# Kernel optimization log

Hardware: AMD Instinct MI355X
Metric: run time of the kernel (lower is better)

The kernel has to match this reference:

```python
import jax, jax.numpy as jnp
import numpy as np

B, S, E, H = 2, 2048, 1024, 16
D = E // H  # head_dim = 64


def setup_inputs() -> dict:
    key = jax.random.key(0)
    ks = jax.random.split(key, 7)
    scale = 1.0 / np.sqrt(E)
    return {
        "q": jax.random.normal(ks[0], (B, S, E), jnp.float32),
        "k": jax.random.normal(ks[1], (B, S, E), jnp.float32),
        "v": jax.random.normal(ks[2], (B, S, E), jnp.float32),
        "Wq": jax.random.normal(ks[3], (E, E), jnp.float32) * scale,
        "bq": jnp.zeros((E,), jnp.float32),
        "Wk": jax.random.normal(ks[4], (E, E), jnp.float32) * scale,
        "bk": jnp.zeros((E,), jnp.float32),
        "Wv": jax.random.normal(ks[5], (E, E), jnp.float32) * scale,
        "bv": jnp.zeros((E,), jnp.float32),
        "Wo": jax.random.normal(ks[6], (E, E), jnp.float32) * scale,
        "bo": jnp.zeros((E,), jnp.float32),
    }


def _split_heads(x):
    # [B, S, E] -> [B, H, S, D]
    b, s, _ = x.shape
    return x.reshape(b, s, H, D).transpose(0, 2, 1, 3)


def reference(q, k, v, Wq, bq, Wk, bk, Wv, bv, Wo, bo):
    qh = _split_heads(q @ Wq + bq)  # [B,H,S,D]
    kh = _split_heads(k @ Wk + bk)
    vh = _split_heads(v @ Wv + bv)
    scores = jnp.einsum("bhqd,bhkd->bhqk", qh, kh) / jnp.sqrt(jnp.float32(D))
    # causal mask, TF band_part(ones, -1, 0) == lower triangular
    mask = jnp.tril(jnp.ones((S, S), jnp.float32))
    scores = scores * mask - 1e9 * (1.0 - mask)
    weights = jax.nn.softmax(scores, axis=-1)
    attn = jnp.einsum("bhqk,bhkd->bhqd", weights, vh)  # [B,H,S,D]
    concat = attn.transpose(0, 2, 1, 3).reshape(q.shape[0], S, E)
    return concat @ Wo + bo
```

## Files before the change

### kernel.cpp

```cpp
#include <hip/hip_runtime.h>
#include <math.h>

#define Bd 2
#define Sd 2048
#define Ed 1024
#define Hd 16
#define Dd 64
#define Md (Bd * Sd)
#define Kd 1024
#define Nd 1024

typedef __attribute__((ext_vector_type(8))) short bf16x8;
typedef __attribute__((ext_vector_type(4))) float f32x4;

__device__ __forceinline__ unsigned short f2bf(float f) {
    unsigned x = __float_as_uint(f);
    x += 0x7fffu + ((x >> 16) & 1u);
    return (unsigned short)(x >> 16);
}

__device__ __forceinline__ unsigned pk_bf16_rhu(float a, float b) {
    return __builtin_amdgcn_perm(__float_as_uint(b) + 0x8000u,
                                 __float_as_uint(a) + 0x8000u, 0x07060302u);
}

__device__ __forceinline__ void gl2lds16(const unsigned short* g, unsigned short* l) {
    __builtin_amdgcn_global_load_lds(
        (__attribute__((address_space(1))) void*)g,
        (__attribute__((address_space(3))) void*)l, 16, 0, 0);
}

__global__ __launch_bounds__(256) void prep_k(
    const float* __restrict__ q, const float* __restrict__ k, const float* __restrict__ v,
    unsigned short* __restrict__ qb, unsigned short* __restrict__ kb,
    unsigned short* __restrict__ vb,
    const float* __restrict__ w0, const float* __restrict__ w1,
    const float* __restrict__ w2, const float* __restrict__ w3,
    unsigned short* __restrict__ o0, unsigned short* __restrict__ o1,
    unsigned short* __restrict__ o2, unsigned short* __restrict__ o3)
{
    const int bx = blockIdx.x;
    if (bx < 3072) {
        const int zz = bx >> 10;
        const int blk = bx & 1023;
        const float* s = zz == 0 ? q : zz == 1 ? k : v;
        unsigned short* d = zz == 0 ? qb : zz == 1 ? kb : vb;
        const int n4 = (Bd * Sd * Ed) / 4;
        int i = blk * 256 + threadIdx.x;
        for (; i < n4; i += 1024 * 256) {
            float4 x = ((const float4*)s)[i];
            uint2 u = make_uint2(pk_bf16_rhu(x.x, x.y), pk_bf16_rhu(x.z, x.w));
            ((uint2*)d)[i] = u;
        }
        return;
    }
    __shared__ unsigned short Tl[32][36];
    const int idx = bx - 3072;
    const int z   = idx >> 10;
    const int ky  = (idx >> 5) & 31;
    const int nx  = idx & 31;
    const float* W = z == 0 ? w0 : z == 1 ? w1 : z == 2 ? w2 : w3;
    unsigned short* Wt = z == 0 ? o0 : z == 1 ? o1 : z == 2 ? o2 : o3;

    const int t = threadIdx.x;
    const int r = t >> 3;
    const int c4 = (t & 7) * 4;
    const int k0 = ky * 32;
    const int n0 = nx * 32;

    float4 x = *(const float4*)(W + (size_t)(k0 + r) * Nd + n0 + c4);
    Tl[c4 + 0][r] = f2bf(x.x);
    Tl[c4 + 1][r] = f2bf(x.y);
    Tl[c4 + 2][r] = f2bf(x.z);
    Tl[c4 + 3][r] = f2bf(x.w);
    __syncthreads();
    ushort4 u = make_ushort4(Tl[r][c4 + 0], Tl[r][c4 + 1], Tl[r][c4 + 2], Tl[r][c4 + 3]);
    *(ushort4*)(Wt + (size_t)(n0 + r) * Kd + k0 + c4) = u;
}

template <int AM>
__device__ __forceinline__ void gemm_v5(
    const unsigned short* __restrict__ A, const unsigned short* __restrict__ Bt,
    const float* __restrict__ bias, void* __restrict__ Yv,
    int m0, int n0, int mode, float oscale)
{
    constexpr int AMT = AM / 32;
    __shared__ unsigned short As[2][AM * 32];
    __shared__ unsigned short Bs[2][128 * 32];

    const int tid  = threadIdx.x;
    const int w    = tid >> 6;
    const int lane = tid & 63;
    const int ln   = lane & 15;
    const int quad = lane >> 4;
    const int wm = (w >> 1) * (AM / 2);
    const int wn = (w & 1) * 64;

    const int lrow = lane >> 2;
    const int lcol = (lane & 3) * 8;

    const unsigned short* Bg0 = Bt + (size_t)(n0 + (2 * w) * 16 + lrow) * Kd + lcol;
    const unsigned short* Bg1 = Bg0 + 16 * Kd;
    const int aseg = (AM == 128) ? 2 * w : w;
    const unsigned short* Ag0 = A + (size_t)(m0 + aseg * 16 + lrow) * Kd + lcol;
    const unsigned short* Ag1 = Ag0 + 16 * Kd;

    f32x4 acc[AMT][4];
    #pragma unroll
    for (int i = 0; i < AMT; ++i)
        #pragma unroll
        for (int j = 0; j < 4; ++j)
            acc[i][j] = (f32x4){0.f, 0.f, 0.f, 0.f};

    gl2lds16(Bg0, &Bs[0][(2 * w) * 512]);
    gl2lds16(Bg1, &Bs[0][(2 * w) * 512 + 512]);
    gl2lds16(Ag0, &As[0][aseg * 512]);
    if constexpr (AM == 128) gl2lds16(Ag1, &As[0][aseg * 512 + 512]);

    for (int k0 = 0; k0 < Kd; k0 += 32) {
        const int buf = (k0 >> 5) & 1;
        __syncthreads();

        if (k0 + 32 < Kd) {
            gl2lds16(Bg0 + k0 + 32, &Bs[buf ^ 1][(2 * w) * 512]);
            gl2lds16(Bg1 + k0 + 32, &Bs[buf ^ 1][(2 * w) * 512 + 512]);
            gl2lds16(Ag0 + k0 + 32, &As[buf ^ 1][aseg * 512]);
            if constexpr (AM == 128)
                gl2lds16(Ag1 + k0 + 32, &As[buf ^ 1][aseg * 512 + 512]);
        }

        bf16x8 af[AMT], bfr[4];
        #pragma unroll
        for (int mi = 0; mi < AMT; ++mi)
            af[mi] = *(const bf16x8*)(&As[buf][(wm + mi * 16 + ln) * 32 + quad * 8]);
        #pragma unroll
        for (int ni = 0; ni < 4; ++ni)
            bfr[ni] = *(const bf16x8*)(&Bs[buf][(wn + ni * 16 + ln) * 32 + quad * 8]);
        #pragma unroll
        for (int mi = 0; mi < AMT; ++mi)
            #pragma unroll
            for (int ni = 0; ni < 4; ++ni)
                acc[mi][ni] = __builtin_amdgcn_mfma_f32_16x16x32_bf16(
                    af[mi], bfr[ni], acc[mi][ni], 0, 0, 0);
    }

    float bval[4];
    #pragma unroll
    for (int ni = 0; ni < 4; ++ni) bval[ni] = bias[n0 + wn + ni * 16 + ln];

    if (mode == 0) {
        float* Y = (float*)Yv;
        #pragma unroll
        for (int mi = 0; mi < AMT; ++mi) {
            #pragma unroll
            for (int ni = 0; ni < 4; ++ni) {
                int n = n0 + wn + ni * 16 + ln;
                #pragma unroll
                for (int r = 0; r < 4; ++r) {
                    int m = m0 + wm + mi * 16 + quad * 4 + r;
                    Y[(size_t)m * Nd + n] = (acc[mi][ni][r] + bval[ni]) * oscale;
                }
            }
        }
    } else if (mode == 1) {
        unsigned short* Y = (unsigned short*)Yv;
        #pragma unroll
        for (int mi = 0; mi < AMT; ++mi) {
            #pragma unroll
            for (int ni = 0; ni < 4; ++ni) {
                int n = n0 + wn + ni * 16 + ln;
                int h = n >> 6, d = n & 63;
                #pragma unroll
                for (int r = 0; r < 4; ++r) {
                    int m = m0 + wm + mi * 16 + quad * 4 + r;
                    int b = m >> 11, s = m & 2047;
                    Y[(((size_t)b * Hd + h) * Sd + s) * Dd + d] =
                        f2bf((acc[mi][ni][r] + bval[ni]) * oscale);
                }
            }
        }
    } else {
        unsigned short* Y = (unsigned short*)Yv;
        #pragma unroll
        for (int mi = 0; mi < AMT; ++mi) {
            int mbase = m0 + wm + mi * 16 + quad * 4;
            int b = mbase >> 11, s = mbase & 2047;
            #pragma unroll
            for (int ni = 0; ni < 4; ++ni) {
                int n = n0 + wn + ni * 16 + ln;
                int h = n >> 6, d = n & 63;
                ushort4 u = make_ushort4(
                    f2bf((acc[mi][ni][0] + bval[ni]) * oscale),
                    f2bf((acc[mi][ni][1] + bval[ni]) * oscale),
                    f2bf((acc[mi][ni][2] + bval[ni]) * oscale),
                    f2bf((acc[mi][ni][3] + bval[ni]) * oscale));
                *(ushort4*)(Y + (((size_t)b * Hd + h) * Dd + d) * Sd + s) = u;
            }
        }
    }
}

__global__ __launch_bounds__(256) void proj_gemm_k(
    const unsigned short* A0, const unsigned short* A1, const unsigned short* A2,
    const unsigned short* B0, const unsigned short* B1, const unsigned short* B2,
    const float* b0, const float* b1, const float* b2,
    unsigned short* Y0, unsigned short* Y1, unsigned short* Y2)
{
    const int l    = blockIdx.x;
    const int xcd  = l & 7;
    const int g    = l >> 3;
    const int n_t  = g & 7;
    const int msub = (g >> 3) & 3;
    const int z    = g >> 5;
    const int m_t  = xcd * 4 + msub;

    const unsigned short* A = z == 0 ? A0 : z == 1 ? A1 : A2;
    const unsigned short* B = z == 0 ? B0 : z == 1 ? B1 : B2;
    const float* bias       = z == 0 ? b0 : z == 1 ? b1 : b2;
    unsigned short* Y       = z == 0 ? Y0 : z == 1 ? Y1 : Y2;
    gemm_v5<128>(A, B, bias, Y, m_t * 128, n_t * 128,
                 z == 2 ? 2 : 1,
                 z == 0 ? 0.18033688011112042f : 1.0f);
}

__global__ __launch_bounds__(256) void out_gemm_k(
    const unsigned short* A, const unsigned short* Bt, const float* bias, float* Y)
{
    const int l    = blockIdx.x;
    const int xcd  = l & 7;
    const int g    = l >> 3;
    const int n_t  = g & 7;
    const int msub = g >> 3;
    const int m_t  = xcd * 8 + msub;
    gemm_v5<64>(A, Bt, bias, Y, m_t * 64, n_t * 128, 0, 1.0f);
}

__global__ __launch_bounds__(256) void attn_mfma_k(
    const unsigned short* __restrict__ Qg,
    const unsigned short* __restrict__ Kg,
    const unsigned short* __restrict__ Vg,
    unsigned short* __restrict__ Aout)
{
    __shared__ unsigned short Ks[2][2][64 * 64];
    __shared__ unsigned short Vs[2][2][64 * 64];
    __shared__ unsigned short Pt[4][16][72];

    const int tid  = threadIdx.x;
    const int w    = tid >> 6;
    const int lane = tid & 63;
    const int ln   = lane & 15;
    const int quad = lane >> 4;

    const int l   = blockIdx.x;
    const int bh  = (l & 7) * 4 + ((l >> 3) & 3);
    const int qtA = l >> 5;
    const int b   = bh >> 4;
    const int h   = bh & 15;

    const size_t baseQK = (size_t)bh * Sd * Dd;
    const size_t baseV  = (size_t)bh * Dd * Sd;
    const f32x4 vzero = {0.f, 0.f, 0.f, 0.f};

    const int qtB = 31 - qtA;
    const int nA  = qtA + 1;

    const int sr = lane >> 3;
    const int sc = ((lane & 7) ^ sr) * 8;
    const int rb0 = w * 16, rb1 = w * 16 + 8;
    const int swl = ln & 7;
    const int c0 = ((quad    ) ^ swl) * 8;
    const int c1 = ((quad + 4) ^ swl) * 8;

    const int qrowA = qtA * 64 + w * 16;
    const int qrowB = qtB * 64 + w * 16;
    const unsigned short* qpA = Qg + baseQK + (size_t)(qrowA + ln) * Dd + 8 * quad;
    const unsigned short* qpB = Qg + baseQK + (size_t)(qrowB + ln) * Dd + 8 * quad;
    const bf16x8 qA0 = *(const bf16x8*)(qpA), qA1 = *(const bf16x8*)(qpA + 32);
    const bf16x8 qB0 = *(const bf16x8*)(qpB), qB1 = *(const bf16x8*)(qpB + 32);

    float l_lane = 0.f;
    f32x4 O[4];
    #pragma unroll
    for (int t = 0; t < 4; ++t) O[t] = vzero;

    #pragma unroll
    for (int s = 0; s < 2; ++s) {
        const int ts = s;
        const int nk = ((ts < nA) ? ts : ts - nA) * 64;
        gl2lds16(Kg + baseQK + (size_t)(nk + rb0 + sr) * Dd + sc, &Ks[0][s][rb0 * 64]);
        gl2lds16(Kg + baseQK + (size_t)(nk + rb1 + sr) * Dd + sc, &Ks[0][s][rb1 * 64]);
        gl2lds16(Vg + baseV  + (size_t)(rb0 + sr) * Sd + nk + sc, &Vs[0][s][rb0 * 64]);
        gl2lds16(Vg + baseV  + (size_t)(rb1 + sr) * Sd + nk + sc, &Vs[0][s][rb1 * 64]);
    }

    for (int g = 0; g < 17; ++g) {
        const int cur = g & 1;
        __syncthreads();

        if (g + 1 < 17) {
            #pragma unroll
            for (int s = 0; s < 2; ++s) {
                const int ts = 2 * (g + 1) + s;
                if (ts < 33) {
                    const int nk = ((ts < nA) ? ts : ts - nA) * 64;
                    gl2lds16(Kg + baseQK + (size_t)(nk + rb0 + sr) * Dd + sc,
                             &Ks[cur ^ 1][s][rb0 * 64]);
                    gl2lds16(Kg + baseQK + (size_t)(nk + rb1 + sr) * Dd + sc,
                             &Ks[cur ^ 1][s][rb1 * 64]);
                    gl2lds16(Vg + baseV  + (size_t)(rb0 + sr) * Sd + nk + sc,
                             &Vs[cur ^ 1][s][rb0 * 64]);
                    gl2lds16(Vg + baseV  + (size_t)(rb1 + sr) * Sd + nk + sc,
                             &Vs[cur ^ 1][s][rb1 * 64]);
                }
            }
        }

        #pragma unroll
        for (int s = 0; s < 2; ++s) {
            const int it = 2 * g + s;
            if (it >= 33) break;

            const bool inA   = (it < nA);
            const int  krow  = (inA ? it : it - nA) * 64;
            const bool diag  = inA ? (it == nA - 1) : (it == 32);
            const int  qglob = (inA ? qrowA : qrowB) + ln;
            const bf16x8 qf0 = inA ? qA0 : qB0;
            const bf16x8 qf1 = inA ? qA1 : qB1;

            f32x4 S[4];
            #pragma unroll
            for (int t = 0; t < 4; ++t) {
                const int R = (t * 16 + ln) * 64;
                bf16x8 k0 = *(const bf16x8*)&Ks[cur][s][R + c0];
                bf16x8 k1 = *(const bf16x8*)&Ks[cur][s][R + c1];
                f32x4 z = __builtin_amdgcn_mfma_f32_16x16x32_bf16(k0, qf0, vzero, 0, 0, 0);
                S[t]     = __builtin_amdgcn_mfma_f32_16x16x32_bf16(k1, qf1, z,     0, 0, 0);
            }

            if (diag) {
                #pragma unroll
                for (int t = 0; t < 4; ++t)
                    #pragma unroll
                    for (int r = 0; r < 4; ++r)
                        if (krow + t * 16 + quad * 4 + r > qglob)
                            S[t][r] = -1e30f;
            }

            float p[16];
            float rsum = 0.f;
            #pragma unroll
            for (int t = 0; t < 4; ++t) {
                #pragma unroll
                for (int r = 0; r < 4; ++r) {
                    float e = __builtin_amdgcn_exp2f(S[t][r]);
                    p[t * 4 + r] = e;
                    rsum += e;
                }
            }
            l_lane += rsum;

            #pragma unroll
            for (int t = 0; t < 4; ++t) {
                uint2 u = make_uint2(pk_bf16_rhu(p[t * 4 + 0], p[t * 4 + 1]),
                                     pk_bf16_rhu(p[t * 4 + 2], p[t * 4 + 3]));
                *(uint2*)&Pt[w][ln][t * 16 + quad * 4] = u;
            }
            bf16x8 pf0 = *(const bf16x8*)&Pt[w][ln][8 * quad];
            bf16x8 pf1 = *(const bf16x8*)&Pt[w][ln][32 + 8 * quad];

            #pragma unroll
            for (int t = 0; t < 4; ++t) {
                const int R = (t * 16 + ln) * 64;
                bf16x8 v0 = *(const bf16x8*)&Vs[cur][s][R + c0];
                bf16x8 v1 = *(const bf16x8*)&Vs[cur][s][R + c1];
                O[t] = __builtin_amdgcn_mfma_f32_16x16x32_bf16(v0, pf0, O[t], 0, 0, 0);
                O[t] = __builtin_amdgcn_mfma_f32_16x16x32_bf16(v1, pf1, O[t], 0, 0, 0);
            }

            if (it == nA - 1) {
                float l_run = l_lane;
                l_run += __shfl_xor(l_run, 16);
                l_run += __shfl_xor(l_run, 32);
                float inv = 1.f / l_run;
                unsigned short* op =
                    Aout + ((size_t)b * Sd + qrowA + ln) * Ed + h * 64 + quad * 4;
                #pragma unroll
                for (int t = 0; t < 4; ++t) {
                    ushort4 u = make_ushort4(f2bf(O[t][0] * inv), f2bf(O[t][1] * inv),
                                             f2bf(O[t][2] * inv), f2bf(O[t][3] * inv));
                    *(ushort4*)(op + t * 16) = u;
                }
                l_lane = 0.f;
                #pragma unroll
                for (int t = 0; t < 4; ++t) O[t] = vzero;
            }
        }
    }

    float l_run = l_lane;
    l_run += __shfl_xor(l_run, 16);
    l_run += __shfl_xor(l_run, 32);
    float inv = 1.f / l_run;
    unsigned short* op = Aout + ((size_t)b * Sd + qrowB + ln) * Ed + h * 64 + quad * 4;
    #pragma unroll
    for (int t = 0; t < 4; ++t) {
        ushort4 u = make_ushort4(f2bf(O[t][0] * inv), f2bf(O[t][1] * inv),
                                 f2bf(O[t][2] * inv), f2bf(O[t][3] * inv));
        *(ushort4*)(op + t * 16) = u;
    }
}

extern "C" void kernel_launch(void* const* d_in, const int* in_sizes, int n_in,
                              void* d_out, int out_size, void* d_ws, size_t ws_size,
                              hipStream_t stream) {
    const float* q  = (const float*)d_in[0];
    const float* k  = (const float*)d_in[1];
    const float* v  = (const float*)d_in[2];
    const float* Wq = (const float*)d_in[3];
    const float* bq = (const float*)d_in[4];
    const float* Wk = (const float*)d_in[5];
    const float* bk = (const float*)d_in[6];
    const float* Wv = (const float*)d_in[7];
    const float* bv = (const float*)d_in[8];
    const float* Wo = (const float*)d_in[9];
    const float* bo = (const float*)d_in[10];

    const size_t TENS = (size_t)Bd * Sd * Ed;
    const size_t WE   = (size_t)Ed * Ed;
    unsigned short* qb  = (unsigned short*)d_ws;
    unsigned short* kb  = qb + TENS;
    unsigned short* vb  = kb + TENS;
    unsigned short* Wqt = vb + TENS;
    unsigned short* Wkt = Wqt + WE;
    unsigned short* Wvt = Wkt + WE;
    unsigned short* Wot = Wvt + WE;
    unsigned short* Qh  = Wot + WE;
    unsigned short* Kh  = Qh + TENS;
    unsigned short* Vt  = Kh + TENS;
    unsigned short* An  = Vt + TENS;

    prep_k<<<dim3(7168), 256, 0, stream>>>(q, k, v, qb, kb, vb,
                                           Wq, Wk, Wv, Wo, Wqt, Wkt, Wvt, Wot);
    proj_gemm_k<<<dim3(768), 256, 0, stream>>>(
        qb, kb, vb, Wqt, Wkt, Wvt, bq, bk, bv, Qh, Kh, Vt);
    attn_mfma_k<<<dim3(512), 256, 0, stream>>>(Qh, Kh, Vt, An);
    out_gemm_k<<<dim3(512), 256, 0, stream>>>(An, Wot, bo, (float*)d_out);
}
```

Measured before the change: 205.0 us.

## Drop LDS K/V staging in attention, load fragments directly from global

The attention kernel no longer stages K/V tiles through double-buffered shared memory with barriers. Each wave now loads its K and V MFMA fragments straight from global memory (through L2/cache). The paired-query-tile scheme that balanced causal work is replaced by one query tile per block with a grid of 1024, ordered heaviest-first, and launch bounds request 4 blocks per CU. The aim is to remove barrier and LDS overhead and raise occupancy, at the cost of four waves redundantly reading the same K/V from cache and less coalesced global loads.

```diff
diff --git a/kernel.cpp b/kernel.cpp
--- a/kernel.cpp
+++ b/kernel.cpp
@@ -235,14 +235,12 @@
     gemm_v5<64>(A, Bt, bias, Y, m_t * 64, n_t * 128, 0, 1.0f);
 }
 
-__global__ __launch_bounds__(256) void attn_mfma_k(
+__global__ __launch_bounds__(256, 4) void attn_mfma_k(
     const unsigned short* __restrict__ Qg,
     const unsigned short* __restrict__ Kg,
     const unsigned short* __restrict__ Vg,
     unsigned short* __restrict__ Aout)
 {
-    __shared__ unsigned short Ks[2][2][64 * 64];
-    __shared__ unsigned short Vs[2][2][64 * 64];
     __shared__ unsigned short Pt[4][16][72];
 
     const int tid  = threadIdx.x;
@@ -253,7 +251,7 @@
 
     const int l   = blockIdx.x;
     const int bh  = (l & 7) * 4 + ((l >> 3) & 3);
-    const int qtA = l >> 5;
+    const int qt  = 31 - (l >> 5);
     const int b   = bh >> 4;
     const int h   = bh & 15;
 
@@ -261,139 +259,80 @@
     const size_t baseV  = (size_t)bh * Dd * Sd;
     const f32x4 vzero = {0.f, 0.f, 0.f, 0.f};
 
-    const int qtB = 31 - qtA;
-    const int nA  = qtA + 1;
-
-    const int sr = lane >> 3;
-    const int sc = ((lane & 7) ^ sr) * 8;
-    const int rb0 = w * 16, rb1 = w * 16 + 8;
-    const int swl = ln & 7;
-    const int c0 = ((quad    ) ^ swl) * 8;
-    const int c1 = ((quad + 4) ^ swl) * 8;
-
-    const int qrowA = qtA * 64 + w * 16;
-    const int qrowB = qtB * 64 + w * 16;
-    const unsigned short* qpA = Qg + baseQK + (size_t)(qrowA + ln) * Dd + 8 * quad;
-    const unsigned short* qpB = Qg + baseQK + (size_t)(qrowB + ln) * Dd + 8 * quad;
-    const bf16x8 qA0 = *(const bf16x8*)(qpA), qA1 = *(const bf16x8*)(qpA + 32);
-    const bf16x8 qB0 = *(const bf16x8*)(qpB), qB1 = *(const bf16x8*)(qpB + 32);
+    const int qrow  = qt * 64 + w * 16;
+    const int qglob = qrow + ln;
+    const unsigned short* qp = Qg + baseQK + (size_t)qglob * Dd + 8 * quad;
+    const bf16x8 q0 = *(const bf16x8*)(qp), q1 = *(const bf16x8*)(qp + 32);
+
+    const unsigned short* Kb = Kg + baseQK + (size_t)ln * Dd + 8 * quad;
+    const unsigned short* Vb = Vg + baseV  + (size_t)ln * Sd + 8 * quad;
 
     float l_lane = 0.f;
     f32x4 O[4];
     #pragma unroll
     for (int t = 0; t < 4; ++t) O[t] = vzero;
 
-    #pragma unroll
-    for (int s = 0; s < 2; ++s) {
-        const int ts = s;
-        const int nk = ((ts < nA) ? ts : ts - nA) * 64;
-        gl2lds16(Kg + baseQK + (size_t)(nk + rb0 + sr) * Dd + sc, &Ks[0][s][rb0 * 64]);
-        gl2lds16(Kg + baseQK + (size_t)(nk + rb1 + sr) * Dd + sc, &Ks[0][s][rb1 * 64]);
-        gl2lds16(Vg + baseV  + (size_t)(rb0 + sr) * Sd + nk + sc, &Vs[0][s][rb0 * 64]);
-        gl2lds16(Vg + baseV  + (size_t)(rb1 + sr) * Sd + nk + sc, &Vs[0][s][rb1 * 64]);
-    }
-
-    for (int g = 0; g < 17; ++g) {
-        const int cur = g & 1;
-        __syncthreads();
-
-        if (g + 1 < 17) {
-            #pragma unroll
-            for (int s = 0; s < 2; ++s) {
-                const int ts = 2 * (g + 1) + s;
-                if (ts < 33) {
-                    const int nk = ((ts < nA) ? ts : ts - nA) * 64;
-                    gl2lds16(Kg + baseQK + (size_t)(nk + rb0 + sr) * Dd + sc,
-                             &Ks[cur ^ 1][s][rb0 * 64]);
-                    gl2lds16(Kg + baseQK + (size_t)(nk + rb1 + sr) * Dd + sc,
-                             &Ks[cur ^ 1][s][rb1 * 64]);
-                    gl2lds16(Vg + baseV  + (size_t)(rb0 + sr) * Sd + nk + sc,
-                             &Vs[cur ^ 1][s][rb0 * 64]);
-                    gl2lds16(Vg + baseV  + (size_t)(rb1 + sr) * Sd + nk + sc,
-                             &Vs[cur ^ 1][s][rb1 * 64]);
-                }
+    for (int it = 0; it <= qt; ++it) {
+        const int nk = it * 64;
+        const unsigned short* kp = Kb + (size_t)nk * Dd;
+        const unsigned short* vp = Vb + nk;
+
+        bf16x8 kf0[4], kf1[4];
+        #pragma unroll
+        for (int t = 0; t < 4; ++t) {
+            kf0[t] = *(const bf16x8*)(kp + t * (16 * Dd));
+            kf1[t] = *(const bf16x8*)(kp + t * (16 * Dd) + 32);
+        }
+
+        f32x4 S[4];
+        #pragma unroll
+        for (int t = 0; t < 4; ++t) {
+            f32x4 z = __builtin_amdgcn_mfma_f32_16x16x32_bf16(kf0[t], q0, vzero, 0, 0, 0);
+            S[t]    = __builtin_amdgcn_mfma_f32_16x16x32_bf16(kf1[t], q1, z,     0, 0, 0);
+        }
+
+        bf16x8 vf0[4], vf1[4];
+        #pragma unroll
+        for (int t = 0; t < 4; ++t) {
+            vf0[t] = *(const bf16x8*)(vp + t * (16 * Sd));
+            vf1[t] = *(const bf16x8*)(vp + t * (16 * Sd) + 32);
+        }
+
+        if (it == qt) {
+            #pragma unroll
+            for (int t = 0; t < 4; ++t)
+                #pragma unroll
+                for (int r = 0; r < 4; ++r)
+                    if (nk + t * 16 + quad * 4 + r > qglob)
+                        S[t][r] = -1e30f;
+        }
+
+        float p[16];
+        float rsum = 0.f;
+        #pragma unroll
+        for (int t = 0; t < 4; ++t) {
+            #pragma unroll
+            for (int r = 0; r < 4; ++r) {
+                float e = __builtin_amdgcn_exp2f(S[t][r]);
+                p[t * 4 + r] = e;
+                rsum += e;
             }
         }
-
-        #pragma unroll
-        for (int s = 0; s < 2; ++s) {
-            const int it = 2 * g + s;
-            if (it >= 33) break;
-
-            const bool inA   = (it < nA);
-            const int  krow  = (inA ? it : it - nA) * 64;
-            const bool diag  = inA ? (it == nA - 1) : (it == 32);
-            const int  qglob = (inA ? qrowA : qrowB) + ln;
-            const bf16x8 qf0 = inA ? qA0 : qB0;
-            const bf16x8 qf1 = inA ? qA1 : qB1;
-
-            f32x4 S[4];
-            #pragma unroll
-            for (int t = 0; t < 4; ++t) {
-                const int R = (t * 16 + ln) * 64;
-                bf16x8 k0 = *(const bf16x8*)&Ks[cur][s][R + c0];
-                bf16x8 k1 = *(const bf16x8*)&Ks[cur][s][R + c1];
-                f32x4 z = __builtin_amdgcn_mfma_f32_16x16x32_bf16(k0, qf0, vzero, 0, 0, 0);
-                S[t]     = __builtin_amdgcn_mfma_f32_16x16x32_bf16(k1, qf1, z,     0, 0, 0);
-            }
-
-            if (diag) {
-                #pragma unroll
-                for (int t = 0; t < 4; ++t)
-                    #pragma unroll
-                    for (int r = 0; r < 4; ++r)
-                        if (krow + t * 16 + quad * 4 + r > qglob)
-                            S[t][r] = -1e30f;
-            }
-
-            float p[16];
-            float rsum = 0.f;
-            #pragma unroll
-            for (int t = 0; t < 4; ++t) {
-                #pragma unroll
-                for (int r = 0; r < 4; ++r) {
-                    float e = __builtin_amdgcn_exp2f(S[t][r]);
-                    p[t * 4 + r] = e;
-                    rsum += e;
-                }
-            }
-            l_lane += rsum;
-
-            #pragma unroll
-            for (int t = 0; t < 4; ++t) {
-                uint2 u = make_uint2(pk_bf16_rhu(p[t * 4 + 0], p[t * 4 + 1]),
-                                     pk_bf16_rhu(p[t * 4 + 2], p[t * 4 + 3]));
-                *(uint2*)&Pt[w][ln][t * 16 + quad * 4] = u;
-            }
-            bf16x8 pf0 = *(const bf16x8*)&Pt[w][ln][8 * quad];
-            bf16x8 pf1 = *(const bf16x8*)&Pt[w][ln][32 + 8 * quad];
-
-            #pragma unroll
-            for (int t = 0; t < 4; ++t) {
-                const int R = (t * 16 + ln) * 64;
-                bf16x8 v0 = *(const bf16x8*)&Vs[cur][s][R + c0];
-                bf16x8 v1 = *(const bf16x8*)&Vs[cur][s][R + c1];
-                O[t] = __builtin_amdgcn_mfma_f32_16x16x32_bf16(v0, pf0, O[t], 0, 0, 0);
-                O[t] = __builtin_amdgcn_mfma_f32_16x16x32_bf16(v1, pf1, O[t], 0, 0, 0);
-            }
-
-            if (it == nA - 1) {
-                float l_run = l_lane;
-                l_run += __shfl_xor(l_run, 16);
-                l_run += __shfl_xor(l_run, 32);
-                float inv = 1.f / l_run;
-                unsigned short* op =
-                    Aout + ((size_t)b * Sd + qrowA + ln) * Ed + h * 64 + quad * 4;
-                #pragma unroll
-                for (int t = 0; t < 4; ++t) {
-                    ushort4 u = make_ushort4(f2bf(O[t][0] * inv), f2bf(O[t][1] * inv),
-                                             f2bf(O[t][2] * inv), f2bf(O[t][3] * inv));
-                    *(ushort4*)(op + t * 16) = u;
-                }
-                l_lane = 0.f;
-                #pragma unroll
-                for (int t = 0; t < 4; ++t) O[t] = vzero;
-            }
+        l_lane += rsum;
+
+        #pragma unroll
+        for (int t = 0; t < 4; ++t) {
+            uint2 u = make_uint2(pk_bf16_rhu(p[t * 4 + 0], p[t * 4 + 1]),
+                                 pk_bf16_rhu(p[t * 4 + 2], p[t * 4 + 3]));
+            *(uint2*)&Pt[w][ln][t * 16 + quad * 4] = u;
+        }
+        bf16x8 pf0 = *(const bf16x8*)&Pt[w][ln][8 * quad];
+        bf16x8 pf1 = *(const bf16x8*)&Pt[w][ln][32 + 8 * quad];
+
+        #pragma unroll
+        for (int t = 0; t < 4; ++t) {
+            O[t] = __builtin_amdgcn_mfma_f32_16x16x32_bf16(vf0[t], pf0, O[t], 0, 0, 0);
+            O[t] = __builtin_amdgcn_mfma_f32_16x16x32_bf16(vf1[t], pf1, O[t], 0, 0, 0);
         }
     }
 
@@ -401,7 +340,7 @@
     l_run += __shfl_xor(l_run, 16);
     l_run += __shfl_xor(l_run, 32);
     float inv = 1.f / l_run;
-    unsigned short* op = Aout + ((size_t)b * Sd + qrowB + ln) * Ed + h * 64 + quad * 4;
+    unsigned short* op = Aout + ((size_t)b * Sd + qglob) * Ed + h * 64 + quad * 4;
     #pragma unroll
     for (int t = 0; t < 4; ++t) {
         ushort4 u = make_ushort4(f2bf(O[t][0] * inv), f2bf(O[t][1] * inv),
@@ -443,6 +382,6 @@
                                            Wq, Wk, Wv, Wo, Wqt, Wkt, Wvt, Wot);
     proj_gemm_k<<<dim3(768), 256, 0, stream>>>(
         qb, kb, vb, Wqt, Wkt, Wvt, bq, bk, bv, Qh, Kh, Vt);
-    attn_mfma_k<<<dim3(512), 256, 0, stream>>>(Qh, Kh, Vt, An);
+    attn_mfma_k<<<dim3(1024), 256, 0, stream>>>(Qh, Kh, Vt, An);
     out_gemm_k<<<dim3(512), 256, 0, stream>>>(An, Wot, bo, (float*)d_out);
 }
```

After: 310.4 us. 51.4% more time.

## Share K/V tiles between paired query tiles in causal attention

Applied to the files above, without the earlier changes.

Previously each block streamed K/V for query tile A and then separately for query tile B, 33 tiles in total. Now the loop runs only over B's key range (qtB+1 tiles), and each loaded K/V tile is used for both query tiles while it is within A's causal range. This cuts global-to-LDS traffic and barrier count, because tiles 0..qtA are loaded once instead of twice. In exchange the block holds two accumulator sets, which raises register pressure. It also creates load imbalance, since per-block work now depends on qtB (between 17 and 32 tile loads) rather than a constant 33.

```diff
diff --git a/kernel.cpp b/kernel.cpp
--- a/kernel.cpp
+++ b/kernel.cpp
@@ -254,6 +254,7 @@
     const int l   = blockIdx.x;
     const int bh  = (l & 7) * 4 + ((l >> 3) & 3);
     const int qtA = l >> 5;
+    const int qtB = 31 - qtA;
     const int b   = bh >> 4;
     const int h   = bh & 15;
 
@@ -261,8 +262,8 @@
     const size_t baseV  = (size_t)bh * Dd * Sd;
     const f32x4 vzero = {0.f, 0.f, 0.f, 0.f};
 
-    const int qtB = 31 - qtA;
-    const int nA  = qtA + 1;
+    const int nsub = qtB + 1;
+    const int ngrp = (nsub + 1) >> 1;
 
     const int sr = lane >> 3;
     const int sc = ((lane & 7) ^ sr) * 8;
@@ -273,44 +274,45 @@
 
     const int qrowA = qtA * 64 + w * 16;
     const int qrowB = qtB * 64 + w * 16;
-    const unsigned short* qpA = Qg + baseQK + (size_t)(qrowA + ln) * Dd + 8 * quad;
-    const unsigned short* qpB = Qg + baseQK + (size_t)(qrowB + ln) * Dd + 8 * quad;
+    const int qgA = qrowA + ln, qgB = qrowB + ln;
+    const unsigned short* qpA = Qg + baseQK + (size_t)qgA * Dd + 8 * quad;
+    const unsigned short* qpB = Qg + baseQK + (size_t)qgB * Dd + 8 * quad;
     const bf16x8 qA0 = *(const bf16x8*)(qpA), qA1 = *(const bf16x8*)(qpA + 32);
     const bf16x8 qB0 = *(const bf16x8*)(qpB), qB1 = *(const bf16x8*)(qpB + 32);
 
-    float l_lane = 0.f;
-    f32x4 O[4];
+    float lA = 0.f, lB = 0.f;
+    f32x4 OA[4], OB[4];
     #pragma unroll
-    for (int t = 0; t < 4; ++t) O[t] = vzero;
+    for (int t = 0; t < 4; ++t) { OA[t] = vzero; OB[t] = vzero; }
+
+    const unsigned short* Kst0 = Kg + baseQK + (size_t)(rb0 + sr) * Dd + sc;
+    const unsigned short* Kst1 = Kg + baseQK + (size_t)(rb1 + sr) * Dd + sc;
+    const unsigned short* Vst0 = Vg + baseV  + (size_t)(rb0 + sr) * Sd + sc;
+    const unsigned short* Vst1 = Vg + baseV  + (size_t)(rb1 + sr) * Sd + sc;
 
     #pragma unroll
     for (int s = 0; s < 2; ++s) {
-        const int ts = s;
-        const int nk = ((ts < nA) ? ts : ts - nA) * 64;
-        gl2lds16(Kg + baseQK + (size_t)(nk + rb0 + sr) * Dd + sc, &Ks[0][s][rb0 * 64]);
-        gl2lds16(Kg + baseQK + (size_t)(nk + rb1 + sr) * Dd + sc, &Ks[0][s][rb1 * 64]);
-        gl2lds16(Vg + baseV  + (size_t)(rb0 + sr) * Sd + nk + sc, &Vs[0][s][rb0 * 64]);
-        gl2lds16(Vg + baseV  + (size_t)(rb1 + sr) * Sd + nk + sc, &Vs[0][s][rb1 * 64]);
-    }
-
-    for (int g = 0; g < 17; ++g) {
+        const int nk = s * 64;
+        gl2lds16(Kst0 + (size_t)nk * Dd, &Ks[0][s][rb0 * 64]);
+        gl2lds16(Kst1 + (size_t)nk * Dd, &Ks[0][s][rb1 * 64]);
+        gl2lds16(Vst0 + nk, &Vs[0][s][rb0 * 64]);
+        gl2lds16(Vst1 + nk, &Vs[0][s][rb1 * 64]);
+    }
+
+    for (int g = 0; g < ngrp; ++g) {
         const int cur = g & 1;
         __syncthreads();
 
-        if (g + 1 < 17) {
+        if (g + 1 < ngrp) {
             #pragma unroll
             for (int s = 0; s < 2; ++s) {
                 const int ts = 2 * (g + 1) + s;
-                if (ts < 33) {
-                    const int nk = ((ts < nA) ? ts : ts - nA) * 64;
-                    gl2lds16(Kg + baseQK + (size_t)(nk + rb0 + sr) * Dd + sc,
-                             &Ks[cur ^ 1][s][rb0 * 64]);
-                    gl2lds16(Kg + baseQK + (size_t)(nk + rb1 + sr) * Dd + sc,
-                             &Ks[cur ^ 1][s][rb1 * 64]);
-                    gl2lds16(Vg + baseV  + (size_t)(rb0 + sr) * Sd + nk + sc,
-                             &Vs[cur ^ 1][s][rb0 * 64]);
-                    gl2lds16(Vg + baseV  + (size_t)(rb1 + sr) * Sd + nk + sc,
-                             &Vs[cur ^ 1][s][rb1 * 64]);
+                if (ts < nsub) {
+                    const int nk = ts * 64;
+                    gl2lds16(Kst0 + (size_t)nk * Dd, &Ks[cur ^ 1][s][rb0 * 64]);
+                    gl2lds16(Kst1 + (size_t)nk * Dd, &Ks[cur ^ 1][s][rb1 * 64]);
+                    gl2lds16(Vst0 + nk, &Vs[cur ^ 1][s][rb0 * 64]);
+                    gl2lds16(Vst1 + nk, &Vs[cur ^ 1][s][rb1 * 64]);
                 }
             }
         }
@@ -318,94 +320,129 @@
         #pragma unroll
         for (int s = 0; s < 2; ++s) {
             const int it = 2 * g + s;
-            if (it >= 33) break;
-
-            const bool inA   = (it < nA);
-            const int  krow  = (inA ? it : it - nA) * 64;
-            const bool diag  = inA ? (it == nA - 1) : (it == 32);
-            const int  qglob = (inA ? qrowA : qrowB) + ln;
-            const bf16x8 qf0 = inA ? qA0 : qB0;
-            const bf16x8 qf1 = inA ? qA1 : qB1;
-
-            f32x4 S[4];
+            if (it >= nsub) break;
+            const int nk  = it * 64;
+            const bool doA = (it <= qtA);
+
+            bf16x8 kf0[4], kf1[4];
             #pragma unroll
             for (int t = 0; t < 4; ++t) {
                 const int R = (t * 16 + ln) * 64;
-                bf16x8 k0 = *(const bf16x8*)&Ks[cur][s][R + c0];
-                bf16x8 k1 = *(const bf16x8*)&Ks[cur][s][R + c1];
-                f32x4 z = __builtin_amdgcn_mfma_f32_16x16x32_bf16(k0, qf0, vzero, 0, 0, 0);
-                S[t]     = __builtin_amdgcn_mfma_f32_16x16x32_bf16(k1, qf1, z,     0, 0, 0);
-            }
-
-            if (diag) {
+                kf0[t] = *(const bf16x8*)&Ks[cur][s][R + c0];
+                kf1[t] = *(const bf16x8*)&Ks[cur][s][R + c1];
+            }
+
+            f32x4 SB[4], SA[4];
+            #pragma unroll
+            for (int t = 0; t < 4; ++t) {
+                f32x4 z = __builtin_amdgcn_mfma_f32_16x16x32_bf16(kf0[t], qB0, vzero, 0, 0, 0);
+                SB[t]   = __builtin_amdgcn_mfma_f32_16x16x32_bf16(kf1[t], qB1, z,     0, 0, 0);
+            }
+            if (doA) {
+                #pragma unroll
+                for (int t = 0; t < 4; ++t) {
+                    f32x4 z = __builtin_amdgcn_mfma_f32_16x16x32_bf16(kf0[t], qA0, vzero, 0, 0, 0);
+                    SA[t]   = __builtin_amdgcn_mfma_f32_16x16x32_bf16(kf1[t], qA1, z,     0, 0, 0);
+                }
+            }
+
+            if (it == qtB) {
                 #pragma unroll
                 for (int t = 0; t < 4; ++t)
                     #pragma unroll
                     for (int r = 0; r < 4; ++r)
-                        if (krow + t * 16 + quad * 4 + r > qglob)
-                            S[t][r] = -1e30f;
-            }
-
-            float p[16];
-            float rsum = 0.f;
-            #pragma unroll
-            for (int t = 0; t < 4; ++t) {
-                #pragma unroll
-                for (int r = 0; r < 4; ++r) {
-                    float e = __builtin_amdgcn_exp2f(S[t][r]);
-                    p[t * 4 + r] = e;
-                    rsum += e;
-                }
-            }
-            l_lane += rsum;
-
-            #pragma unroll
-            for (int t = 0; t < 4; ++t) {
-                uint2 u = make_uint2(pk_bf16_rhu(p[t * 4 + 0], p[t * 4 + 1]),
-                                     pk_bf16_rhu(p[t * 4 + 2], p[t * 4 + 3]));
-                *(uint2*)&Pt[w][ln][t * 16 + quad * 4] = u;
-            }
-            bf16x8 pf0 = *(const bf16x8*)&Pt[w][ln][8 * quad];
-            bf16x8 pf1 = *(const bf16x8*)&Pt[w][ln][32 + 8 * quad];
+                        if (nk + t * 16 + quad * 4 + r > qgB)
+                            SB[t][r] = -1e30f;
+            }
+            if (doA && it == qtA) {
+                #pragma unroll
+                for (int t = 0; t < 4; ++t)
+                    #pragma unroll
+                    for (int r = 0; r < 4; ++r)
+                        if (nk + t * 16 + quad * 4 + r > qgA)
+                            SA[t][r] = -1e30f;
+            }
+
+            {
+                float p[16]; float rsum = 0.f;
+                #pragma unroll
+                for (int t = 0; t < 4; ++t)
+                    #pragma unroll
+                    for (int r = 0; r < 4; ++r) {
+                        float e = __builtin_amdgcn_exp2f(SB[t][r]);
+                        p[t * 4 + r] = e; rsum += e;
+                    }
+                lB += rsum;
+                #pragma unroll
+                for (int t = 0; t < 4; ++t) {
+                    uint2 u = make_uint2(pk_bf16_rhu(p[t * 4 + 0], p[t * 4 + 1]),
+                                         pk_bf16_rhu(p[t * 4 + 2], p[t * 4 + 3]));
+                    *(uint2*)&Pt[w][ln][t * 16 + quad * 4] = u;
+                }
+            }
+            const bf16x8 pfB0 = *(const bf16x8*)&Pt[w][ln][8 * quad];
+            const bf16x8 pfB1 = *(const bf16x8*)&Pt[w][ln][32 + 8 * quad];
+
+            bf16x8 pfA0, pfA1;
+            if (doA) {
+                float p[16]; float rsum = 0.f;
+                #pragma unroll
+                for (int t = 0; t < 4; ++t)
+                    #pragma unroll
+                    for (int r = 0; r < 4; ++r) {
+                        float e = __builtin_amdgcn_exp2f(SA[t][r]);
+                        p[t * 4 + r] = e; rsum += e;
+                    }
+                lA += rsum;
+                #pragma unroll
+                for (int t = 0; t < 4; ++t) {
+                    uint2 u = make_uint2(pk_bf16_rhu(p[t * 4 + 0], p[t * 4 + 1]),
+                                         pk_bf16_rhu(p[t * 4 + 2], p[t * 4 + 3]));
+                    *(uint2*)&Pt[w][ln][t * 16 + quad * 4] = u;
+                }
+                pfA0 = *(const bf16x8*)&Pt[w][ln][8 * quad];
+                pfA1 = *(const bf16x8*)&Pt[w][ln][32 + 8 * quad];
+            }
 
             #pragma unroll
             for (int t = 0; t < 4; ++t) {
                 const int R = (t * 16 + ln) * 64;
                 bf16x8 v0 = *(const bf16x8*)&Vs[cur][s][R + c0];
                 bf16x8 v1 = *(const bf16x8*)&Vs[cur][s][R + c1];
-                O[t] = __builtin_amdgcn_mfma_f32_16x16x32_bf16(v0, pf0, O[t], 0, 0, 0);
-                O[t] = __builtin_amdgcn_mfma_f32_16x16x32_bf16(v1, pf1, O[t], 0, 0, 0);
-            }
-
-            if (it == nA - 1) {
-                float l_run = l_lane;
+                OB[t] = __builtin_amdgcn_mfma_f32_16x16x32_bf16(v0, pfB0, OB[t], 0, 0, 0);
+                OB[t] = __builtin_amdgcn_mfma_f32_16x16x32_bf16(v1, pfB1, OB[t], 0, 0, 0);
+                if (doA) {
+                    OA[t] = __builtin_amdgcn_mfma_f32_16x16x32_bf16(v0, pfA0, OA[t], 0, 0, 0);
+                    OA[t] = __builtin_amdgcn_mfma_f32_16x16x32_bf16(v1, pfA1, OA[t], 0, 0, 0);
+                }
+            }
+
+            if (doA && it == qtA) {
+                float l_run = lA;
                 l_run += __shfl_xor(l_run, 16);
                 l_run += __shfl_xor(l_run, 32);
                 float inv = 1.f / l_run;
                 unsigned short* op =
-                    Aout + ((size_t)b * Sd + qrowA + ln) * Ed + h * 64 + quad * 4;
+                    Aout + ((size_t)b * Sd + qgA) * Ed + h * 64 + quad * 4;
                 #pragma unroll
                 for (int t = 0; t < 4; ++t) {
-                    ushort4 u = make_ushort4(f2bf(O[t][0] * inv), f2bf(O[t][1] * inv),
-                                             f2bf(O[t][2] * inv), f2bf(O[t][3] * inv));
+                    ushort4 u = make_ushort4(f2bf(OA[t][0] * inv), f2bf(OA[t][1] * inv),
+                                             f2bf(OA[t][2] * inv), f2bf(OA[t][3] * inv));
                     *(ushort4*)(op + t * 16) = u;
                 }
-                l_lane = 0.f;
-                #pragma unroll
-                for (int t = 0; t < 4; ++t) O[t] = vzero;
-            }
-        }
-    }
-
-    float l_run = l_lane;
+            }
+        }
+    }
+
+    float l_run = lB;
     l_run += __shfl_xor(l_run, 16);
     l_run += __shfl_xor(l_run, 32);
     float inv = 1.f / l_run;
-    unsigned short* op = Aout + ((size_t)b * Sd + qrowB + ln) * Ed + h * 64 + quad * 4;
+    unsigned short* op = Aout + ((size_t)b * Sd + qgB) * Ed + h * 64 + quad * 4;
     #pragma unroll
     for (int t = 0; t < 4; ++t) {
-        ushort4 u = make_ushort4(f2bf(O[t][0] * inv), f2bf(O[t][1] * inv),
-                                 f2bf(O[t][2] * inv), f2bf(O[t][3] * inv));
+        ushort4 u = make_ushort4(f2bf(OB[t][0] * inv), f2bf(OB[t][1] * inv),
+                                 f2bf(OB[t][2] * inv), f2bf(OB[t][3] * inv));
         *(ushort4*)(op + t * 16) = u;
     }
 }
```

Result: no change. 208.0 us (+1.4%).
